# Kernel tuning notes

Hardware: AMD Instinct MI355X
Metric: run time of the kernel (lower is better)

## Reference

```python
import jax, jax.numpy as jnp
import numpy as np

N_NODES = 50000
N_EDGES = 1200000
N_GRAPHS = 512
GC_COUNT = 3
CUTOFF = 8.0
BN_EPS = 1e-5
LOG2 = float(np.log(2.0))


def ssp(v):
    # ShiftedSoftplus
    return jax.nn.softplus(v) - LOG2


def setup_inputs() -> dict:
    key = jax.random.key(0)
    ks = jax.random.split(key, 16)
    d1, nf, ng = 64, 92, 50
    inp = {}
    inp["x"] = jax.random.normal(ks[0], (N_NODES, nf), dtype=jnp.float32)
    # distances in [0, cutoff)
    inp["edge_weight"] = jax.random.uniform(ks[1], (N_EDGES,), dtype=jnp.float32) * CUTOFF
    inp["edge_attr"] = jax.random.normal(ks[2], (N_EDGES, ng), dtype=jnp.float32)
    inp["edge_index"] = jax.random.randint(ks[3], (2, N_EDGES), 0, N_NODES, dtype=jnp.int32)
    inp["batch"] = jnp.sort(jax.random.randint(ks[4], (N_NODES,), 0, N_GRAPHS, dtype=jnp.int32))
    s = lambda fan_in: 1.0 / np.sqrt(fan_in)
    inp["pre_W"] = jax.random.normal(ks[5], (d1, nf), dtype=jnp.float32) * s(nf)
    inp["pre_b"] = jnp.zeros((d1,), jnp.float32)
    inp["mlp_W1"] = jax.random.normal(ks[6], (GC_COUNT, d1, ng), dtype=jnp.float32) * s(ng)
    inp["mlp_b1"] = jnp.zeros((GC_COUNT, d1), jnp.float32)
    inp["mlp_W2"] = jax.random.normal(ks[7], (GC_COUNT, d1, d1), dtype=jnp.float32) * s(d1)
    inp["mlp_b2"] = jnp.zeros((GC_COUNT, d1), jnp.float32)
    inp["cf_W1"] = jax.random.normal(ks[8], (GC_COUNT, d1, d1), dtype=jnp.float32) * s(d1)
    inp["cf_W2"] = jax.random.normal(ks[9], (GC_COUNT, d1, d1), dtype=jnp.float32) * s(d1)
    inp["cf_b2"] = jnp.zeros((GC_COUNT, d1), jnp.float32)
    inp["int_W"] = jax.random.normal(ks[10], (GC_COUNT, d1, d1), dtype=jnp.float32) * s(d1)
    inp["int_b"] = jnp.zeros((GC_COUNT, d1), jnp.float32)
    inp["bn_g"] = jnp.ones((GC_COUNT, d1), jnp.float32)
    inp["bn_b"] = jnp.zeros((GC_COUNT, d1), jnp.float32)
    inp["post_W"] = jax.random.normal(ks[11], (d1, d1), dtype=jnp.float32) * s(d1)
    inp["post_b"] = jnp.zeros((d1,), jnp.float32)
    inp["out_W"] = jax.random.normal(ks[12], (1, d1), dtype=jnp.float32) * s(d1)
    inp["out_b"] = jnp.zeros((1,), jnp.float32)
    return inp


def reference(x, edge_weight, edge_attr, edge_index, batch,
              pre_W, pre_b, mlp_W1, mlp_b1, mlp_W2, mlp_b2,
              cf_W1, cf_W2, cf_b2, int_W, int_b, bn_g, bn_b,
              post_W, post_b, out_W, out_b):
    src, dst = edge_index[0], edge_index[1]
    # pre FC
    out = jax.nn.relu(x @ pre_W.T + pre_b)
    # cosine cutoff on edge distances, shared across layers
    C = 0.5 * (jnp.cos(edge_weight * (jnp.pi / CUTOFF)) + 1.0)  # [E]
    for l in range(GC_COUNT):
        # filter-generating MLP on edge_attr, modulated by cutoff
        W = ssp(edge_attr @ mlp_W1[l].T + mlp_b1[l]) @ mlp_W2[l].T + mlp_b2[l]
        W = W * C[:, None]  # [E, F]
        # CFConv: lin1 -> gather -> modulate -> scatter-add -> lin2
        h = out @ cf_W1[l].T                      # [N, F]
        msg = h[src] * W                          # [E, F]
        agg = jax.ops.segment_sum(msg, dst, num_segments=N_NODES)  # [N, F]
        h = agg @ cf_W2[l].T + cf_b2[l]
        # InteractionBlock tail: act + lin
        h = ssp(h) @ int_W[l].T + int_b[l]
        out = out + h
        # BatchNorm1d (training mode: batch statistics, biased variance)
        mu = jnp.mean(out, axis=0)
        var = jnp.mean((out - mu) ** 2, axis=0)
        out = (out - mu) * jax.lax.rsqrt(var + BN_EPS) * bn_g[l] + bn_b[l]
    # global_mean_pool over graphs
    sums = jax.ops.segment_sum(out, batch, num_segments=N_GRAPHS)  # [G, F]
    counts = jax.ops.segment_sum(jnp.ones((out.shape[0],), out.dtype), batch, num_segments=N_GRAPHS)
    pooled = sums / jnp.maximum(counts, 1.0)[:, None]
    # post FC + head
    h = jax.nn.relu(pooled @ post_W.T + post_b)
    y = h @ out_W.T + out_b  # [G, 1]
    return y.reshape(-1)
```

## Files before the change

kernel.cpp:

```cpp
#include <hip/hip_runtime.h>

constexpr int N = 50000;
constexpr int E = 1200000;
constexpr int G = 512;
constexpr int TILES = E / 64;
constexpr float LOG2_ = 0.69314718055994531f;
constexpr float PIC = 0.39269908169872414f;

__device__ __forceinline__ float sspf(float x) {
    return fmaxf(x, 0.f) + __logf(1.f + __expf(-fabsf(x))) - LOG2_;
}
__device__ __forceinline__ void uadd(float* p, float v) { unsafeAtomicAdd(p, v); }

__global__ __launch_bounds__(256) void k_hist(const int* __restrict__ eidx,
                                              int* __restrict__ cnt) {
    for (int e = blockIdx.x * 256 + threadIdx.x; e < E; e += gridDim.x * 256)
        atomicAdd(cnt + eidx[E + e], 1);
}

__global__ __launch_bounds__(1024) void k_scan(const int* __restrict__ cnt,
                                               int* __restrict__ cursor) {
    __shared__ int part[1024];
    const int CH = 49;
    int t = threadIdx.x;
    int b = t * CH;
    int s = 0;
    for (int i = 0; i < CH; i++) { int idx = b + i; if (idx < N) s += cnt[idx]; }
    part[t] = s;
    __syncthreads();
    for (int off = 1; off < 1024; off <<= 1) {
        int add = (t >= off) ? part[t - off] : 0;
        int v = part[t];
        __syncthreads();
        part[t] = v + add;
        __syncthreads();
    }
    int excl = (t == 0) ? 0 : part[t - 1];
    for (int i = 0; i < CH; i++) {
        int idx = b + i;
        if (idx < N) { cursor[idx] = excl; excl += cnt[idx]; }
    }
}

__global__ __launch_bounds__(256) void k_scatter(const int* __restrict__ eidx,
                                                 int* __restrict__ cursor,
                                                 int* __restrict__ order) {
    for (int e = blockIdx.x * 256 + threadIdx.x; e < E; e += gridDim.x * 256) {
        int d = eidx[E + e];
        int p = atomicAdd(cursor + d, 1);
        order[p] = e;
    }
}

__global__ __launch_bounds__(256) void k_pre(const float* __restrict__ x,
                                             const float* __restrict__ W,
                                             const float* __restrict__ b,
                                             float* __restrict__ out) {
    __shared__ float WT[92 * 64];
    __shared__ float xs[4 * 92];
    __shared__ float bs[64];
    for (int i = threadIdx.x; i < 92 * 64; i += 256) {
        int f = i / 92, k = i - f * 92;
        WT[k * 64 + f] = W[i];
    }
    if (threadIdx.x < 64) bs[threadIdx.x] = b[threadIdx.x];
    __syncthreads();
    int f = threadIdx.x & 63, nl = threadIdx.x >> 6;
    for (int g0 = blockIdx.x; g0 < N / 4; g0 += gridDim.x) {
        int n0 = g0 * 4;
        for (int i = threadIdx.x; i < 4 * 92; i += 256) xs[i] = x[(size_t)n0 * 92 + i];
        __syncthreads();
        float acc = bs[f];
        #pragma unroll 4
        for (int k = 0; k < 92; k++) acc = fmaf(xs[nl * 92 + k], WT[k * 64 + f], acc);
        out[(size_t)(n0 + nl) * 64 + f] = fmaxf(acc, 0.f);
        __syncthreads();
    }
}

__global__ __launch_bounds__(256) void k_h(const float* __restrict__ out,
                                           const float* __restrict__ W,
                                           float* __restrict__ h) {
    __shared__ float WT[64 * 64];
    __shared__ float xs[4 * 64];
    for (int i = threadIdx.x; i < 4096; i += 256) {
        int f = i >> 6, j = i & 63;
        WT[j * 64 + f] = W[i];
    }
    __syncthreads();
    int f = threadIdx.x & 63, nl = threadIdx.x >> 6;
    for (int g0 = blockIdx.x; g0 < N / 4; g0 += gridDim.x) {
        int n0 = g0 * 4;
        if (threadIdx.x < 64)
            ((float4*)xs)[threadIdx.x] = ((const float4*)(out + (size_t)n0 * 64))[threadIdx.x];
        __syncthreads();
        float acc = 0.f;
        #pragma unroll 4
        for (int j = 0; j < 64; j++) acc = fmaf(xs[nl * 64 + j], WT[j * 64 + f], acc);
        h[(size_t)(n0 + nl) * 64 + f] = acc;
        __syncthreads();
    }
}

__global__ __launch_bounds__(256) void k_edge(const float* __restrict__ ea,
                                              const float* __restrict__ ew,
                                              const int* __restrict__ eidx,
                                              const int* __restrict__ order,
                                              const float* __restrict__ h,
                                              float* __restrict__ agg,
                                              const float* __restrict__ W1,
                                              const float* __restrict__ b1,
                                              const float* __restrict__ W2,
                                              const float* __restrict__ b2) {
    constexpr int BS = 68;
    __shared__ float w1T[50 * 64];
    __shared__ float w2T[64 * 64];
    __shared__ float buf[64 * BS];
    __shared__ float b1s[64], b2s[64], c_s[64];
    __shared__ int src_s[64], dst_s[64], ord_s[64];
    int t = threadIdx.x;
    for (int i = t; i < 3200; i += 256) { int f = i / 50, k = i - f * 50; w1T[k * 64 + f] = W1[i]; }
    for (int i = t; i < 4096; i += 256) { int f = i >> 6, j = i & 63; w2T[j * 64 + f] = W2[i]; }
    if (t < 64) { b1s[t] = b1[t]; b2s[t] = b2[t]; }
    __syncthreads();

    const int e4 = (t & 15) * 4;
    const int f4 = (t >> 4) * 4;
    const int fe = t & 63, kq = t >> 6;

    for (int tile = blockIdx.x; tile < TILES; tile += gridDim.x) {
        const int e0 = tile * 64;
        if (t < 64) {
            int e = order[e0 + t];
            ord_s[t] = e;
            src_s[t] = eidx[e];
            dst_s[t] = eidx[E + e];
            c_s[t] = 0.5f * (__cosf(ew[e] * PIC) + 1.0f);
        }
        __syncthreads();
        {
            const float2* row2 = (const float2*)ea + (size_t)ord_s[fe] * 25;
            #pragma unroll
            for (int j = 0; j < 24; j += 4) {
                int kp = j + kq;
                float2 v = row2[kp];
                buf[(2 * kp) * BS + fe] = v.x;
                buf[(2 * kp + 1) * BS + fe] = v.y;
            }
            if (kq == 0) {
                float2 v = row2[24];
                buf[48 * BS + fe] = v.x;
                buf[49 * BS + fe] = v.y;
            }
        }
        __syncthreads();
        float a[4][4];
        #pragma unroll
        for (int i = 0; i < 4; i++)
            #pragma unroll
            for (int j = 0; j < 4; j++) a[i][j] = b1s[f4 + j];
        #pragma unroll 2
        for (int k = 0; k < 50; k++) {
            float4 av = *(const float4*)&buf[k * BS + e4];
            float4 wv = *(const float4*)&w1T[k * 64 + f4];
            float avv[4] = {av.x, av.y, av.z, av.w};
            float wvv[4] = {wv.x, wv.y, wv.z, wv.w};
            #pragma unroll
            for (int i = 0; i < 4; i++)
                #pragma unroll
                for (int j = 0; j < 4; j++) a[i][j] = fmaf(avv[i], wvv[j], a[i][j]);
        }
        #pragma unroll
        for (int i = 0; i < 4; i++)
            #pragma unroll
            for (int j = 0; j < 4; j++) a[i][j] = sspf(a[i][j]);
        __syncthreads();
        #pragma unroll
        for (int j = 0; j < 4; j++)
            *(float4*)&buf[(f4 + j) * BS + e4] = make_float4(a[0][j], a[1][j], a[2][j], a[3][j]);
        __syncthreads();
        float w[4][4];
        #pragma unroll
        for (int i = 0; i < 4; i++)
            #pragma unroll
            for (int j = 0; j < 4; j++) w[i][j] = b2s[f4 + j];
        #pragma unroll 2
        for (int k = 0; k < 64; k++) {
            float4 tv = *(const float4*)&buf[k * BS + e4];
            float4 wv = *(const float4*)&w2T[k * 64 + f4];
            float tvv[4] = {tv.x, tv.y, tv.z, tv.w};
            float wvv[4] = {wv.x, wv.y, wv.z, wv.w};
            #pragma unroll
            for (int i = 0; i < 4; i++)
                #pragma unroll
                for (int j = 0; j < 4; j++) w[i][j] = fmaf(tvv[i], wvv[j], w[i][j]);
        }
        float4 m[4];
        #pragma unroll
        for (int i = 0; i < 4; i++) {
            int eg = e4 + i;
            float Cv = c_s[eg];
            float4 hv = *(const float4*)&h[(size_t)src_s[eg] * 64 + f4];
            m[i] = make_float4(hv.x * w[i][0] * Cv, hv.y * w[i][1] * Cv,
                               hv.z * w[i][2] * Cv, hv.w * w[i][3] * Cv);
        }
        __syncthreads();
        #pragma unroll
        for (int i = 0; i < 4; i++)
            *(float4*)&buf[(e4 + i) * BS + f4] = m[i];
        __syncthreads();
        #pragma unroll
        for (int i = 0; i < 4; i++) {
            int e = e4 + i;
            int d = dst_s[e];
            if (e > 0 && dst_s[e - 1] == d) continue;
            int end = e + 1;
            while (end < 64 && dst_s[end] == d) end++;
            float4 s = *(const float4*)&buf[e * BS + f4];
            for (int r = e + 1; r < end; r++) {
                const float4 v = *(const float4*)&buf[r * BS + f4];
                s.x += v.x; s.y += v.y; s.z += v.z; s.w += v.w;
            }
            float* ap = agg + (size_t)d * 64 + f4;
            if (e > 0 && end < 64) {
                *(float4*)ap = s;
            } else {
                uadd(ap + 0, s.x); uadd(ap + 1, s.y);
                uadd(ap + 2, s.z); uadd(ap + 3, s.w);
            }
        }
        __syncthreads();
    }
}

__global__ __launch_bounds__(256) void k_post(const float* __restrict__ agg,
                                              const float* __restrict__ W2c,
                                              const float* __restrict__ b2c,
                                              const float* __restrict__ Wi,
                                              const float* __restrict__ bi,
                                              float* __restrict__ out,
                                              float* __restrict__ bnacc) {
    __shared__ float w2T[64 * 64];
    __shared__ float wiT[64 * 64];
    __shared__ float aL[16 * 64];
    __shared__ float sL[16 * 64];
    __shared__ float b2s[64], bis[64];
    int t = threadIdx.x;
    for (int i = t; i < 4096; i += 256) {
        int f = i >> 6, j = i & 63;
        w2T[j * 64 + f] = W2c[i];
        wiT[j * 64 + f] = Wi[i];
    }
    if (t < 64) { b2s[t] = b2c[t]; bis[t] = bi[t]; }
    __syncthreads();
    const int nl = t >> 4;
    const int f4 = (t & 15) * 4;
    for (int g0 = blockIdx.x; g0 < N / 16; g0 += gridDim.x) {
        int n0 = g0 * 16;
        ((float4*)aL)[t] = ((const float4*)(agg + (size_t)n0 * 64))[t];
        __syncthreads();
        float s[4] = {b2s[f4], b2s[f4 + 1], b2s[f4 + 2], b2s[f4 + 3]};
        #pragma unroll 4
        for (int j = 0; j < 64; j++) {
            float av = aL[nl * 64 + j];
            float4 wv = *(const float4*)&w2T[j * 64 + f4];
            s[0] = fmaf(av, wv.x, s[0]);
            s[1] = fmaf(av, wv.y, s[1]);
            s[2] = fmaf(av, wv.z, s[2]);
            s[3] = fmaf(av, wv.w, s[3]);
        }
        #pragma unroll
        for (int j = 0; j < 4; j++) s[j] = sspf(s[j]);
        *(float4*)&sL[nl * 64 + f4] = make_float4(s[0], s[1], s[2], s[3]);
        __syncthreads();
        float h2[4] = {bis[f4], bis[f4 + 1], bis[f4 + 2], bis[f4 + 3]};
        #pragma unroll 4
        for (int j = 0; j < 64; j++) {
            float sv = sL[nl * 64 + j];
            float4 wv = *(const float4*)&wiT[j * 64 + f4];
            h2[0] = fmaf(sv, wv.x, h2[0]);
            h2[1] = fmaf(sv, wv.y, h2[1]);
            h2[2] = fmaf(sv, wv.z, h2[2]);
            h2[3] = fmaf(sv, wv.w, h2[3]);
        }
        float4 ov = *(const float4*)&out[(size_t)(n0 + nl) * 64 + f4];
        ov.x += h2[0]; ov.y += h2[1]; ov.z += h2[2]; ov.w += h2[3];
        *(float4*)&out[(size_t)(n0 + nl) * 64 + f4] = ov;
        *(float4*)&aL[nl * 64 + f4] = ov;
        __syncthreads();
        if (t < 64) {
            float sm = 0.f, s2 = 0.f;
            #pragma unroll 4
            for (int n = 0; n < 16; n++) {
                float v = aL[n * 64 + t];
                sm += v;
                s2 = fmaf(v, v, s2);
            }
            uadd(bnacc + t, sm);
            uadd(bnacc + 64 + t, s2);
        }
        __syncthreads();
    }
}

__global__ void k_bnfin(float* bnacc, const float* __restrict__ g, const float* __restrict__ b) {
    int f = threadIdx.x;
    double mu = (double)bnacc[f] / (double)N;
    double var = (double)bnacc[64 + f] / (double)N - mu * mu;
    double inv = 1.0 / sqrt(var + 1e-5);
    double sc = (double)g[f] * inv;
    bnacc[128 + f] = (float)sc;
    bnacc[192 + f] = (float)((double)b[f] - mu * sc);
}

__global__ __launch_bounds__(256) void k_bnapply(float* __restrict__ out,
                                                 const float* __restrict__ bnacc) {
    int idx = blockIdx.x * 256 + threadIdx.x;
    int j = idx & 15;
    float4 sc = ((const float4*)(bnacc + 128))[j];
    float4 sh = ((const float4*)(bnacc + 192))[j];
    float4 v = ((float4*)out)[idx];
    v.x = fmaf(v.x, sc.x, sh.x);
    v.y = fmaf(v.y, sc.y, sh.y);
    v.z = fmaf(v.z, sc.z, sh.z);
    v.w = fmaf(v.w, sc.w, sh.w);
    ((float4*)out)[idx] = v;
}

__global__ __launch_bounds__(256) void k_pool(const float* __restrict__ out,
                                              const int* __restrict__ batch,
                                              float* __restrict__ psum,
                                              float* __restrict__ pcnt) {
    int t = threadIdx.x;
    int q = blockIdx.x * 16 + (t >> 4);
    if (q >= N / 4) return;
    int c = t & 15;
    int n0 = q * 4;
    int gprev = batch[n0];
    float4 acc = {0.f, 0.f, 0.f, 0.f};
    float cnt = 0.f;
    for (int i = 0; i < 4; i++) {
        int n = n0 + i;
        int gb = batch[n];
        float4 v = ((const float4*)(out + (size_t)n * 64))[c];
        if (gb != gprev) {
            float* p = psum + (size_t)gprev * 64 + c * 4;
            uadd(p + 0, acc.x); uadd(p + 1, acc.y); uadd(p + 2, acc.z); uadd(p + 3, acc.w);
            if (c == 0) uadd(pcnt + gprev, cnt);
            acc = make_float4(0.f, 0.f, 0.f, 0.f);
            cnt = 0.f;
            gprev = gb;
        }
        acc.x += v.x; acc.y += v.y; acc.z += v.z; acc.w += v.w;
        cnt += 1.f;
    }
    float* p = psum + (size_t)gprev * 64 + c * 4;
    uadd(p + 0, acc.x); uadd(p + 1, acc.y); uadd(p + 2, acc.z); uadd(p + 3, acc.w);
    if (c == 0) uadd(pcnt + gprev, cnt);
}

__global__ __launch_bounds__(256) void k_head(const float* __restrict__ psum,
                                              const float* __restrict__ pcnt,
                                              const float* __restrict__ pW,
                                              const float* __restrict__ pb,
                                              const float* __restrict__ oW,
                                              const float* __restrict__ ob,
                                              float* __restrict__ y) {
    __shared__ float pl[4][64];
    int t = threadIdx.x;
    int gl = t >> 6, f = t & 63;
    int g = blockIdx.x * 4 + gl;
    float cnt = fmaxf(pcnt[g], 1.f);
    pl[gl][f] = psum[(size_t)g * 64 + f] / cnt;
    __syncthreads();
    float acc = pb[f];
    #pragma unroll 4
    for (int j = 0; j < 64; j++) acc = fmaf(pl[gl][j], pW[f * 64 + j], acc);
    float hh = fmaxf(acc, 0.f);
    float part = hh * oW[f];
    #pragma unroll
    for (int off = 32; off; off >>= 1) part += __shfl_xor(part, off);
    if (f == 0) y[g] = part + ob[0];
}

extern "C" void kernel_launch(void* const* d_in, const int* in_sizes, int n_in,
                              void* d_out, int out_size, void* d_ws, size_t ws_size,
                              hipStream_t stream) {
    const float* x      = (const float*)d_in[0];
    const float* ew     = (const float*)d_in[1];
    const float* ea     = (const float*)d_in[2];
    const int*   eidx   = (const int*)d_in[3];
    const int*   batch  = (const int*)d_in[4];
    const float* pre_W  = (const float*)d_in[5];
    const float* pre_b  = (const float*)d_in[6];
    const float* mlp_W1 = (const float*)d_in[7];
    const float* mlp_b1 = (const float*)d_in[8];
    const float* mlp_W2 = (const float*)d_in[9];
    const float* mlp_b2 = (const float*)d_in[10];
    const float* cf_W1  = (const float*)d_in[11];
    const float* cf_W2  = (const float*)d_in[12];
    const float* cf_b2  = (const float*)d_in[13];
    const float* int_W  = (const float*)d_in[14];
    const float* int_b  = (const float*)d_in[15];
    const float* bn_g   = (const float*)d_in[16];
    const float* bn_b   = (const float*)d_in[17];
    const float* post_W = (const float*)d_in[18];
    const float* post_b = (const float*)d_in[19];
    const float* out_W  = (const float*)d_in[20];
    const float* out_b  = (const float*)d_in[21];

    float* ws    = (float*)d_ws;
    float* outb  = ws;
    float* hb    = ws + (size_t)N * 64;
    float* aggb  = ws + (size_t)2 * N * 64;
    float* bnacc = ws + (size_t)3 * N * 64;
    float* psum  = bnacc + 256;
    float* pcnt  = psum + (size_t)G * 64;
    int*   cnt   = (int*)(pcnt + G);
    int*   curs  = cnt + N;
    int*   order = curs + N;

    hipMemsetAsync(cnt, 0, (size_t)N * sizeof(int), stream);
    k_hist<<<1024, 256, 0, stream>>>(eidx, cnt);
    k_scan<<<1, 1024, 0, stream>>>(cnt, curs);
    k_scatter<<<2048, 256, 0, stream>>>(eidx, curs, order);

    k_pre<<<1024, 256, 0, stream>>>(x, pre_W, pre_b, outb);

    for (int l = 0; l < 3; l++) {
        hipMemsetAsync(aggb, 0, (size_t)N * 64 * sizeof(float), stream);
        hipMemsetAsync(bnacc, 0, 128 * sizeof(float), stream);
        k_h<<<1024, 256, 0, stream>>>(outb, cf_W1 + l * 4096, hb);
        k_edge<<<1536, 256, 0, stream>>>(ea, ew, eidx, order, hb, aggb,
                                         mlp_W1 + l * 3200, mlp_b1 + l * 64,
                                         mlp_W2 + l * 4096, mlp_b2 + l * 64);
        k_post<<<1024, 256, 0, stream>>>(aggb, cf_W2 + l * 4096, cf_b2 + l * 64,
                                         int_W + l * 4096, int_b + l * 64, outb, bnacc);
        k_bnfin<<<1, 64, 0, stream>>>(bnacc, bn_g + l * 64, bn_b + l * 64);
        k_bnapply<<<3125, 256, 0, stream>>>(outb, bnacc);
    }

    hipMemsetAsync(psum, 0, (size_t)(G * 64 + G) * sizeof(float), stream);
    k_pool<<<(N / 4 + 15) / 16, 256, 0, stream>>>(outb, batch, psum, pcnt);
    k_head<<<G / 4, 256, 0, stream>>>(psum, pcnt, post_W, post_b, out_W, out_b, (float*)d_out);
}
```

Before: 2.525 ms.

## Use split-bf16 MFMA for edge MLP, prefetch tiles, fuse BN apply

The edge filter MLP moves from scalar FP32 FMAs to MFMA bf16 instructions. Each operand is split into high and low bf16 parts, so three MFMAs per product keep close to FP32 accuracy. Edge metadata (src, dst, cutoff weight) is precomputed once in sorted order, weights are prepacked, and the next tile's edge_attr is prefetched into registers and double-buffered while the current tile computes. The separate BatchNorm-apply kernel is removed and folded into the next layer's k_h load and into pooling. This adds extra workspace and register pressure, with a small loss of precision from the split-bf16 approximation.

New measurement: 2.775 ms. +9.9%, slower.

```diff
diff --git a/kernel.cpp b/kernel.cpp
--- a/kernel.cpp
+++ b/kernel.cpp
@@ -7,10 +7,20 @@
 constexpr float LOG2_ = 0.69314718055994531f;
 constexpr float PIC = 0.39269908169872414f;
 
+typedef __attribute__((ext_vector_type(8))) short s8;
+typedef __attribute__((ext_vector_type(4))) float f32x4;
+
 __device__ __forceinline__ float sspf(float x) {
     return fmaxf(x, 0.f) + __logf(1.f + __expf(-fabsf(x))) - LOG2_;
 }
 __device__ __forceinline__ void uadd(float* p, float v) { unsafeAtomicAdd(p, v); }
+__device__ __forceinline__ ushort bf16rne(float x) {
+    unsigned u = __float_as_uint(x);
+    return (ushort)((u + 0x7FFFu + ((u >> 16) & 1u)) >> 16);
+}
+__device__ __forceinline__ float bf2f(ushort h) {
+    return __uint_as_float(((unsigned)h) << 16);
+}
 
 __global__ __launch_bounds__(256) void k_hist(const int* __restrict__ eidx,
                                               int* __restrict__ cnt) {
@@ -52,6 +62,39 @@
     }
 }
 
+__global__ __launch_bounds__(256) void k_meta(const int* __restrict__ eidx,
+                                              const float* __restrict__ ew,
+                                              const int* __restrict__ order,
+                                              int* __restrict__ srcs,
+                                              int* __restrict__ dsts,
+                                              float* __restrict__ Cs) {
+    for (int p = blockIdx.x * 256 + threadIdx.x; p < E; p += gridDim.x * 256) {
+        int e = order[p];
+        srcs[p] = eidx[e];
+        dsts[p] = eidx[E + e];
+        Cs[p] = 0.5f * (cosf(ew[e] * PIC) + 1.0f);
+    }
+}
+
+__global__ __launch_bounds__(256) void k_pack(const float* __restrict__ W1,
+                                              const float* __restrict__ W2,
+                                              ushort* __restrict__ wpk) {
+    int l = blockIdx.x;
+    ushort* o = wpk + l * 16384;
+    for (int idx = threadIdx.x; idx < 4096; idx += 256) {
+        int j = idx & 7, f = (idx >> 3) & 63, g = (idx >> 9) & 3, ks = idx >> 11;
+        int k = ks * 32 + g * 8 + j;
+        float v1 = (k < 50) ? W1[l * 3200 + f * 50 + k] : 0.f;
+        ushort h1 = bf16rne(v1);
+        o[idx] = h1;
+        o[4096 + idx] = bf16rne(v1 - bf2f(h1));
+        float v2 = W2[l * 4096 + f * 64 + k];
+        ushort h2 = bf16rne(v2);
+        o[8192 + idx] = h2;
+        o[12288 + idx] = bf16rne(v2 - bf2f(h2));
+    }
+}
+
 __global__ __launch_bounds__(256) void k_pre(const float* __restrict__ x,
                                              const float* __restrict__ W,
                                              const float* __restrict__ b,
@@ -78,21 +121,37 @@
     }
 }
 
-__global__ __launch_bounds__(256) void k_h(const float* __restrict__ out,
+__global__ __launch_bounds__(256) void k_h(float* __restrict__ out,
                                            const float* __restrict__ W,
+                                           const float* __restrict__ bnacc,
+                                           int useBN,
                                            float* __restrict__ h) {
     __shared__ float WT[64 * 64];
     __shared__ float xs[4 * 64];
-    for (int i = threadIdx.x; i < 4096; i += 256) {
+    int t = threadIdx.x;
+    for (int i = t; i < 4096; i += 256) {
         int f = i >> 6, j = i & 63;
         WT[j * 64 + f] = W[i];
     }
+    float4 sc = make_float4(1.f, 1.f, 1.f, 1.f);
+    float4 sh = make_float4(0.f, 0.f, 0.f, 0.f);
+    if (t < 64 && useBN) {
+        sc = ((const float4*)(bnacc + 128))[t & 15];
+        sh = ((const float4*)(bnacc + 192))[t & 15];
+    }
     __syncthreads();
-    int f = threadIdx.x & 63, nl = threadIdx.x >> 6;
+    int f = t & 63, nl = t >> 6;
     for (int g0 = blockIdx.x; g0 < N / 4; g0 += gridDim.x) {
         int n0 = g0 * 4;
-        if (threadIdx.x < 64)
-            ((float4*)xs)[threadIdx.x] = ((const float4*)(out + (size_t)n0 * 64))[threadIdx.x];
+        if (t < 64) {
+            float4 v = ((const float4*)(out + (size_t)n0 * 64))[t];
+            v.x = fmaf(v.x, sc.x, sh.x);
+            v.y = fmaf(v.y, sc.y, sh.y);
+            v.z = fmaf(v.z, sc.z, sh.z);
+            v.w = fmaf(v.w, sc.w, sh.w);
+            ((float4*)xs)[t] = v;
+            if (useBN) ((float4*)(out + (size_t)n0 * 64))[t] = v;
+        }
         __syncthreads();
         float acc = 0.f;
         #pragma unroll 4
@@ -102,123 +161,222 @@
     }
 }
 
-__global__ __launch_bounds__(256) void k_edge(const float* __restrict__ ea,
-                                              const float* __restrict__ ew,
-                                              const int* __restrict__ eidx,
-                                              const int* __restrict__ order,
-                                              const float* __restrict__ h,
-                                              float* __restrict__ agg,
-                                              const float* __restrict__ W1,
-                                              const float* __restrict__ b1,
-                                              const float* __restrict__ W2,
-                                              const float* __restrict__ b2) {
-    constexpr int BS = 68;
-    __shared__ float w1T[50 * 64];
-    __shared__ float w2T[64 * 64];
-    __shared__ float buf[64 * BS];
-    __shared__ float b1s[64], b2s[64], c_s[64];
-    __shared__ int src_s[64], dst_s[64], ord_s[64];
-    int t = threadIdx.x;
-    for (int i = t; i < 3200; i += 256) { int f = i / 50, k = i - f * 50; w1T[k * 64 + f] = W1[i]; }
-    for (int i = t; i < 4096; i += 256) { int f = i >> 6, j = i & 63; w2T[j * 64 + f] = W2[i]; }
-    if (t < 64) { b1s[t] = b1[t]; b2s[t] = b2[t]; }
+__global__ __launch_bounds__(256, 2) void k_edge(const float* __restrict__ ea,
+                                                 const int* __restrict__ order,
+                                                 const int* __restrict__ srcs,
+                                                 const int* __restrict__ dsts,
+                                                 const float* __restrict__ Cs,
+                                                 const float* __restrict__ h,
+                                                 float* __restrict__ agg,
+                                                 const ushort* __restrict__ wpk_l,
+                                                 const float* __restrict__ b1,
+                                                 const float* __restrict__ b2) {
+    __shared__ ushort eaH[64 * 64], eaL[64 * 64];
+    __shared__ ushort t1H[64 * 64], t1L[64 * 64];
+    __shared__ float  bufB[64 * 68];
+    __shared__ int   srcM[2][64];
+    __shared__ int   dstM[2][64];
+    __shared__ float cM[2][64];
+
+    const int t = threadIdx.x;
+    const int w = t >> 6, l = t & 63;
+    const int lm = l & 15, lg = l >> 4;
+
+    s8 b1h[4][2], b1l[4][2], b2h[4][2], b2l[4][2];
+    #pragma unroll
+    for (int ft = 0; ft < 4; ft++)
+        #pragma unroll
+        for (int ks = 0; ks < 2; ks++) {
+            int idx = ((ks * 4 + lg) * 64 + ft * 16 + lm) * 8;
+            b1h[ft][ks] = *(const s8*)(wpk_l + idx);
+            b1l[ft][ks] = *(const s8*)(wpk_l + 4096 + idx);
+            b2h[ft][ks] = *(const s8*)(wpk_l + 8192 + idx);
+            b2l[ft][ks] = *(const s8*)(wpk_l + 12288 + idx);
+        }
+    float b1v[4], b2v[4];
+    #pragma unroll
+    for (int ft = 0; ft < 4; ft++) { b1v[ft] = b1[ft * 16 + lm]; b2v[ft] = b2[ft * 16 + lm]; }
+
+    const int gstride = gridDim.x;
+    const int se = t & 63;
+    const int sq = t >> 6;
+    const int e4 = (t & 15) * 4, f4 = (t >> 4) * 4;
+
+    {
+        int e0 = blockIdx.x * 64;
+        int ord = order[e0 + se];
+        const float* row = ea + (size_t)ord * 50;
+        float pv[16];
+        if (sq < 3) {
+            #pragma unroll
+            for (int i = 0; i < 8; i++) {
+                float2 v = *(const float2*)(row + sq * 16 + i * 2);
+                pv[2 * i] = v.x; pv[2 * i + 1] = v.y;
+            }
+        } else {
+            float2 v = *(const float2*)(row + 48);
+            pv[0] = v.x; pv[1] = v.y;
+            #pragma unroll
+            for (int i = 2; i < 16; i++) pv[i] = 0.f;
+        }
+        #pragma unroll
+        for (int c2 = 0; c2 < 2; c2++) {
+            int swz = (sq * 2 + c2) ^ (se & 7);
+            s8 hi, lo;
+            #pragma unroll
+            for (int j = 0; j < 8; j++) {
+                float x = pv[c2 * 8 + j];
+                ushort hh = bf16rne(x);
+                hi[j] = (short)hh;
+                lo[j] = (short)bf16rne(x - bf2f(hh));
+            }
+            *(s8*)&eaH[se * 64 + swz * 8] = hi;
+            *(s8*)&eaL[se * 64 + swz * 8] = lo;
+        }
+        if (t < 64) srcM[0][t] = srcs[e0 + t];
+        else if (t < 128) dstM[0][t - 64] = dsts[e0 + (t - 64)];
+        else if (t < 192) cM[0][t - 128] = Cs[e0 + (t - 128)];
+    }
     __syncthreads();
 
-    const int e4 = (t & 15) * 4;
-    const int f4 = (t >> 4) * 4;
-    const int fe = t & 63, kq = t >> 6;
-
-    for (int tile = blockIdx.x; tile < TILES; tile += gridDim.x) {
-        const int e0 = tile * 64;
-        if (t < 64) {
-            int e = order[e0 + t];
-            ord_s[t] = e;
-            src_s[t] = eidx[e];
-            dst_s[t] = eidx[E + e];
-            c_s[t] = 0.5f * (__cosf(ew[e] * PIC) + 1.0f);
-        }
-        __syncthreads();
+    int it = 0;
+    for (int tile = blockIdx.x; tile < TILES; tile += gstride, it ^= 1) {
+        const int cur = it, nxtb = it ^ 1;
+        int ntile = tile + gstride;
+        int en0 = (ntile < TILES ? ntile : tile) * 64;
+
+        float pv[16];
         {
-            const float2* row2 = (const float2*)ea + (size_t)ord_s[fe] * 25;
-            #pragma unroll
-            for (int j = 0; j < 24; j += 4) {
-                int kp = j + kq;
-                float2 v = row2[kp];
-                buf[(2 * kp) * BS + fe] = v.x;
-                buf[(2 * kp + 1) * BS + fe] = v.y;
-            }
-            if (kq == 0) {
-                float2 v = row2[24];
-                buf[48 * BS + fe] = v.x;
-                buf[49 * BS + fe] = v.y;
-            }
-        }
-        __syncthreads();
-        float a[4][4];
-        #pragma unroll
-        for (int i = 0; i < 4; i++)
-            #pragma unroll
-            for (int j = 0; j < 4; j++) a[i][j] = b1s[f4 + j];
-        #pragma unroll 2
-        for (int k = 0; k < 50; k++) {
-            float4 av = *(const float4*)&buf[k * BS + e4];
-            float4 wv = *(const float4*)&w1T[k * 64 + f4];
-            float avv[4] = {av.x, av.y, av.z, av.w};
-            float wvv[4] = {wv.x, wv.y, wv.z, wv.w};
-            #pragma unroll
-            for (int i = 0; i < 4; i++)
+            int ord = order[en0 + se];
+            const float* row = ea + (size_t)ord * 50;
+            if (sq < 3) {
                 #pragma unroll
-                for (int j = 0; j < 4; j++) a[i][j] = fmaf(avv[i], wvv[j], a[i][j]);
-        }
-        #pragma unroll
-        for (int i = 0; i < 4; i++)
-            #pragma unroll
-            for (int j = 0; j < 4; j++) a[i][j] = sspf(a[i][j]);
-        __syncthreads();
-        #pragma unroll
-        for (int j = 0; j < 4; j++)
-            *(float4*)&buf[(f4 + j) * BS + e4] = make_float4(a[0][j], a[1][j], a[2][j], a[3][j]);
-        __syncthreads();
-        float w[4][4];
-        #pragma unroll
-        for (int i = 0; i < 4; i++)
-            #pragma unroll
-            for (int j = 0; j < 4; j++) w[i][j] = b2s[f4 + j];
-        #pragma unroll 2
-        for (int k = 0; k < 64; k++) {
-            float4 tv = *(const float4*)&buf[k * BS + e4];
-            float4 wv = *(const float4*)&w2T[k * 64 + f4];
-            float tvv[4] = {tv.x, tv.y, tv.z, tv.w};
-            float wvv[4] = {wv.x, wv.y, wv.z, wv.w};
-            #pragma unroll
-            for (int i = 0; i < 4; i++)
+                for (int i = 0; i < 8; i++) {
+                    float2 v = *(const float2*)(row + sq * 16 + i * 2);
+                    pv[2 * i] = v.x; pv[2 * i + 1] = v.y;
+                }
+            } else {
+                float2 v = *(const float2*)(row + 48);
+                pv[0] = v.x; pv[1] = v.y;
                 #pragma unroll
-                for (int j = 0; j < 4; j++) w[i][j] = fmaf(tvv[i], wvv[j], w[i][j]);
-        }
-        float4 m[4];
-        #pragma unroll
-        for (int i = 0; i < 4; i++) {
-            int eg = e4 + i;
-            float Cv = c_s[eg];
-            float4 hv = *(const float4*)&h[(size_t)src_s[eg] * 64 + f4];
-            m[i] = make_float4(hv.x * w[i][0] * Cv, hv.y * w[i][1] * Cv,
-                               hv.z * w[i][2] * Cv, hv.w * w[i][3] * Cv);
-        }
-        __syncthreads();
-        #pragma unroll
-        for (int i = 0; i < 4; i++)
-            *(float4*)&buf[(e4 + i) * BS + f4] = m[i];
-        __syncthreads();
+                for (int i = 2; i < 16; i++) pv[i] = 0.f;
+            }
+        }
+        int pSrc = 0, pDst = 0; float pC = 0.f;
+        if (t < 64) pSrc = srcs[en0 + t];
+        else if (t < 128) pDst = dsts[en0 + (t - 64)];
+        else if (t < 192) pC = Cs[en0 + (t - 128)];
+
+        const int erow = w * 16 + lm;
+        f32x4 acc[4];
+        #pragma unroll
+        for (int ft = 0; ft < 4; ft++) acc[ft] = (f32x4){b1v[ft], b1v[ft], b1v[ft], b1v[ft]};
+        #pragma unroll
+        for (int ks = 0; ks < 2; ks++) {
+            int swz = (ks * 4 + lg) ^ (erow & 7);
+            s8 ah = *(const s8*)&eaH[erow * 64 + swz * 8];
+            s8 al = *(const s8*)&eaL[erow * 64 + swz * 8];
+            #pragma unroll
+            for (int ft = 0; ft < 4; ft++) {
+                acc[ft] = __builtin_amdgcn_mfma_f32_16x16x32_bf16(ah, b1h[ft][ks], acc[ft], 0, 0, 0);
+                acc[ft] = __builtin_amdgcn_mfma_f32_16x16x32_bf16(ah, b1l[ft][ks], acc[ft], 0, 0, 0);
+                acc[ft] = __builtin_amdgcn_mfma_f32_16x16x32_bf16(al, b1h[ft][ks], acc[ft], 0, 0, 0);
+            }
+        }
+        #pragma unroll
+        for (int ft = 0; ft < 4; ft++) {
+            int k = ft * 16 + lm;
+            int cbase = k >> 3;
+            #pragma unroll
+            for (int r = 0; r < 4; r++) {
+                int eR = w * 16 + lg * 4 + r;
+                float v = sspf(acc[ft][r]);
+                ushort hh = bf16rne(v);
+                ushort ll = bf16rne(v - bf2f(hh));
+                int idx = eR * 64 + ((cbase ^ (eR & 7)) << 3) + (k & 7);
+                t1H[idx] = hh;
+                t1L[idx] = ll;
+            }
+        }
+        __syncthreads();
+
+        #pragma unroll
+        for (int c2 = 0; c2 < 2; c2++) {
+            int swz = (sq * 2 + c2) ^ (se & 7);
+            s8 hi, lo;
+            #pragma unroll
+            for (int j = 0; j < 8; j++) {
+                float x = pv[c2 * 8 + j];
+                ushort hh = bf16rne(x);
+                hi[j] = (short)hh;
+                lo[j] = (short)bf16rne(x - bf2f(hh));
+            }
+            *(s8*)&eaH[se * 64 + swz * 8] = hi;
+            *(s8*)&eaL[se * 64 + swz * 8] = lo;
+        }
+        if (t < 64) srcM[nxtb][t] = pSrc;
+        else if (t < 128) dstM[nxtb][t - 64] = pDst;
+        else if (t < 192) cM[nxtb][t - 128] = pC;
+
+        f32x4 acc2[4];
+        #pragma unroll
+        for (int ft = 0; ft < 4; ft++) acc2[ft] = (f32x4){b2v[ft], b2v[ft], b2v[ft], b2v[ft]};
+        #pragma unroll
+        for (int ks = 0; ks < 2; ks++) {
+            int swz = (ks * 4 + lg) ^ (erow & 7);
+            s8 ah = *(const s8*)&t1H[erow * 64 + swz * 8];
+            s8 al = *(const s8*)&t1L[erow * 64 + swz * 8];
+            #pragma unroll
+            for (int ft = 0; ft < 4; ft++) {
+                acc2[ft] = __builtin_amdgcn_mfma_f32_16x16x32_bf16(ah, b2h[ft][ks], acc2[ft], 0, 0, 0);
+                acc2[ft] = __builtin_amdgcn_mfma_f32_16x16x32_bf16(ah, b2l[ft][ks], acc2[ft], 0, 0, 0);
+                acc2[ft] = __builtin_amdgcn_mfma_f32_16x16x32_bf16(al, b2h[ft][ks], acc2[ft], 0, 0, 0);
+            }
+        }
+        float cv[4];
+        #pragma unroll
+        for (int r = 0; r < 4; r++) cv[r] = cM[cur][w * 16 + lg * 4 + r];
+        #pragma unroll
+        for (int ft = 0; ft < 4; ft++) {
+            int f = ft * 16 + lm;
+            #pragma unroll
+            for (int r = 0; r < 4; r++) {
+                int eR = w * 16 + lg * 4 + r;
+                bufB[eR * 68 + f] = acc2[ft][r] * cv[r];
+            }
+        }
+        __syncthreads();
+
+        {
+            int s0 = srcM[cur][e4 + 0], s1 = srcM[cur][e4 + 1];
+            int s2 = srcM[cur][e4 + 2], s3 = srcM[cur][e4 + 3];
+            float4 h0 = *(const float4*)&h[(size_t)s0 * 64 + f4];
+            float4 h1 = *(const float4*)&h[(size_t)s1 * 64 + f4];
+            float4 h2 = *(const float4*)&h[(size_t)s2 * 64 + f4];
+            float4 h3 = *(const float4*)&h[(size_t)s3 * 64 + f4];
+            float4* p0 = (float4*)&bufB[(e4 + 0) * 68 + f4];
+            float4* p1 = (float4*)&bufB[(e4 + 1) * 68 + f4];
+            float4* p2 = (float4*)&bufB[(e4 + 2) * 68 + f4];
+            float4* p3 = (float4*)&bufB[(e4 + 3) * 68 + f4];
+            float4 m0 = *p0, m1 = *p1, m2 = *p2, m3 = *p3;
+            m0.x *= h0.x; m0.y *= h0.y; m0.z *= h0.z; m0.w *= h0.w;
+            m1.x *= h1.x; m1.y *= h1.y; m1.z *= h1.z; m1.w *= h1.w;
+            m2.x *= h2.x; m2.y *= h2.y; m2.z *= h2.z; m2.w *= h2.w;
+            m3.x *= h3.x; m3.y *= h3.y; m3.z *= h3.z; m3.w *= h3.w;
+            *p0 = m0; *p1 = m1; *p2 = m2; *p3 = m3;
+        }
+        __syncthreads();
+
         #pragma unroll
         for (int i = 0; i < 4; i++) {
             int e = e4 + i;
-            int d = dst_s[e];
-            if (e > 0 && dst_s[e - 1] == d) continue;
+            int d = dstM[cur][e];
+            if (e > 0 && dstM[cur][e - 1] == d) continue;
             int end = e + 1;
-            while (end < 64 && dst_s[end] == d) end++;
-            float4 s = *(const float4*)&buf[e * BS + f4];
+            while (end < 64 && dstM[cur][end] == d) end++;
+            float4 s = *(const float4*)&bufB[e * 68 + f4];
             for (int r = e + 1; r < end; r++) {
-                const float4 v = *(const float4*)&buf[r * BS + f4];
+                float4 v = *(const float4*)&bufB[r * 68 + f4];
                 s.x += v.x; s.y += v.y; s.z += v.z; s.w += v.w;
             }
             float* ap = agg + (size_t)d * 64 + f4;
@@ -229,7 +387,6 @@
                 uadd(ap + 2, s.z); uadd(ap + 3, s.w);
             }
         }
-        __syncthreads();
     }
 }
 
@@ -313,28 +470,17 @@
     bnacc[192 + f] = (float)((double)b[f] - mu * sc);
 }
 
-__global__ __launch_bounds__(256) void k_bnapply(float* __restrict__ out,
-                                                 const float* __restrict__ bnacc) {
-    int idx = blockIdx.x * 256 + threadIdx.x;
-    int j = idx & 15;
-    float4 sc = ((const float4*)(bnacc + 128))[j];
-    float4 sh = ((const float4*)(bnacc + 192))[j];
-    float4 v = ((float4*)out)[idx];
-    v.x = fmaf(v.x, sc.x, sh.x);
-    v.y = fmaf(v.y, sc.y, sh.y);
-    v.z = fmaf(v.z, sc.z, sh.z);
-    v.w = fmaf(v.w, sc.w, sh.w);
-    ((float4*)out)[idx] = v;
-}
-
 __global__ __launch_bounds__(256) void k_pool(const float* __restrict__ out,
                                               const int* __restrict__ batch,
+                                              const float* __restrict__ bnacc,
                                               float* __restrict__ psum,
                                               float* __restrict__ pcnt) {
     int t = threadIdx.x;
     int q = blockIdx.x * 16 + (t >> 4);
     if (q >= N / 4) return;
     int c = t & 15;
+    float4 sc = ((const float4*)(bnacc + 128))[c];
+    float4 sh = ((const float4*)(bnacc + 192))[c];
     int n0 = q * 4;
     int gprev = batch[n0];
     float4 acc = {0.f, 0.f, 0.f, 0.f};
@@ -343,6 +489,10 @@
         int n = n0 + i;
         int gb = batch[n];
         float4 v = ((const float4*)(out + (size_t)n * 64))[c];
+        v.x = fmaf(v.x, sc.x, sh.x);
+        v.y = fmaf(v.y, sc.y, sh.y);
+        v.z = fmaf(v.z, sc.z, sh.z);
+        v.w = fmaf(v.w, sc.w, sh.w);
         if (gb != gprev) {
             float* p = psum + (size_t)gprev * 64 + c * 4;
             uadd(p + 0, acc.x); uadd(p + 1, acc.y); uadd(p + 2, acc.z); uadd(p + 3, acc.w);
@@ -419,28 +569,32 @@
     int*   cnt   = (int*)(pcnt + G);
     int*   curs  = cnt + N;
     int*   order = curs + N;
+    int*   srcs  = order + E;
+    int*   dsts  = srcs + E;
+    float* Csrt  = (float*)(dsts + E);
+    ushort* wpk  = (ushort*)(Csrt + E);
 
     hipMemsetAsync(cnt, 0, (size_t)N * sizeof(int), stream);
     k_hist<<<1024, 256, 0, stream>>>(eidx, cnt);
     k_scan<<<1, 1024, 0, stream>>>(cnt, curs);
     k_scatter<<<2048, 256, 0, stream>>>(eidx, curs, order);
+    k_meta<<<2048, 256, 0, stream>>>(eidx, ew, order, srcs, dsts, Csrt);
+    k_pack<<<3, 256, 0, stream>>>(mlp_W1, mlp_W2, wpk);
 
     k_pre<<<1024, 256, 0, stream>>>(x, pre_W, pre_b, outb);
 
     for (int l = 0; l < 3; l++) {
         hipMemsetAsync(aggb, 0, (size_t)N * 64 * sizeof(float), stream);
+        k_h<<<1024, 256, 0, stream>>>(outb, cf_W1 + l * 4096, bnacc, l > 0 ? 1 : 0, hb);
         hipMemsetAsync(bnacc, 0, 128 * sizeof(float), stream);
-        k_h<<<1024, 256, 0, stream>>>(outb, cf_W1 + l * 4096, hb);
-        k_edge<<<1536, 256, 0, stream>>>(ea, ew, eidx, order, hb, aggb,
-                                         mlp_W1 + l * 3200, mlp_b1 + l * 64,
-                                         mlp_W2 + l * 4096, mlp_b2 + l * 64);
+        k_edge<<<512, 256, 0, stream>>>(ea, order, srcs, dsts, Csrt, hb, aggb,
+                                        wpk + l * 16384, mlp_b1 + l * 64, mlp_b2 + l * 64);
         k_post<<<1024, 256, 0, stream>>>(aggb, cf_W2 + l * 4096, cf_b2 + l * 64,
                                          int_W + l * 4096, int_b + l * 64, outb, bnacc);
         k_bnfin<<<1, 64, 0, stream>>>(bnacc, bn_g + l * 64, bn_b + l * 64);
-        k_bnapply<<<3125, 256, 0, stream>>>(outb, bnacc);
     }
 
     hipMemsetAsync(psum, 0, (size_t)(G * 64 + G) * sizeof(float), stream);
-    k_pool<<<(N / 4 + 15) / 16, 256, 0, stream>>>(outb, batch, psum, pcnt);
+    k_pool<<<(N / 4 + 15) / 16, 256, 0, stream>>>(outb, batch, bnacc, psum, pcnt);
     k_head<<<G / 4, 256, 0, stream>>>(psum, pcnt, post_W, post_b, out_W, out_b, (float*)d_out);
 }
```
